# Performance work log

Measured on AMD Instinct MI355X. Metric: run time of the kernel, lower is better.

The kernel has to match this reference:

```python
import jax, jax.numpy as jnp
import numpy as np

B, T, C, H, DH, L, V = 4096, 32, 384, 6, 64, 6, 80


def _ln(x, g, b):
    m = x.mean(-1, keepdims=True)
    v = ((x - m) ** 2).mean(-1, keepdims=True)
    return (x - m) / jnp.sqrt(v + 1e-5) * g + b


def setup_inputs() -> dict:
    key = jax.random.key(0)
    ks = jax.random.split(key, 12)
    n = lambda k, s: jax.random.normal(k, s, dtype=jnp.float32) * 0.02
    return dict(
        idx=jax.random.randint(ks[0], (B, T), 0, V),
        tok_emb=n(ks[1], (V, C)),
        pos_emb=n(ks[2], (T, C)),
        ln1_g=jnp.ones((L, C), jnp.float32), ln1_b=jnp.zeros((L, C), jnp.float32),
        Wq=n(ks[3], (L, H, C, DH)), Wk=n(ks[4], (L, H, C, DH)), Wv=n(ks[5], (L, H, C, DH)),
        Wo=n(ks[6], (L, C, C)), bo=jnp.zeros((L, C), jnp.float32),
        ln2_g=jnp.ones((L, C), jnp.float32), ln2_b=jnp.zeros((L, C), jnp.float32),
        W1=n(ks[7], (L, C, 4 * C)), b1=jnp.zeros((L, 4 * C), jnp.float32),
        W2=n(ks[8], (L, 4 * C, C)), b2=jnp.zeros((L, C), jnp.float32),
        lnf_g=jnp.ones((C,), jnp.float32), lnf_b=jnp.zeros((C,), jnp.float32),
        Wlm=n(ks[9], (C, V)), blm=jnp.zeros((V,), jnp.float32),
    )


def reference(idx, tok_emb, pos_emb, ln1_g, ln1_b, Wq, Wk, Wv, Wo, bo,
              ln2_g, ln2_b, W1, b1, W2, b2, lnf_g, lnf_b, Wlm, blm):
    # token + position embeddings
    x = tok_emb[idx] + pos_emb[None]  # [B, T, C]
    mask = jnp.tril(jnp.ones((T, T), dtype=bool))  # causal

    def block(x, p):
        l1g, l1b, wq, wk, wv, wo, b_o, l2g, l2b, w1, b_1, w2, b_2 = p
        h = _ln(x, l1g, l1b)
        q = jnp.einsum('btc,hcd->bhtd', h, wq)
        k = jnp.einsum('btc,hcd->bhtd', h, wk)
        v = jnp.einsum('btc,hcd->bhtd', h, wv)
        s = jnp.einsum('bhtd,bhsd->bhts', q, k) * (DH ** -0.5)
        s = jnp.where(mask, s, -jnp.inf)
        a = jax.nn.softmax(s, axis=-1)  # dropout is identity in eval
        o = jnp.einsum('bhts,bhsd->bhtd', a, v)
        o = o.transpose(0, 2, 1, 3).reshape(x.shape[0], T, C)  # concat heads
        x = x + o @ wo + b_o
        h2 = _ln(x, l2g, l2b)
        x = x + jax.nn.relu(h2 @ w1 + b_1) @ w2 + b_2
        return x, None

    params = (ln1_g, ln1_b, Wq, Wk, Wv, Wo, bo, ln2_g, ln2_b, W1, b1, W2, b2)
    x, _ = jax.lax.scan(block, x, params)
    x = _ln(x, lnf_g, lnf_b)
    return x @ Wlm + blm  # [B, T, V]
```

## Files before the change

### kernel.cpp

```cpp
#include <hip/hip_runtime.h>
#include <hip/hip_fp16.h>
#include <stdint.h>


typedef unsigned short u16;
typedef __bf16 bf16x8 __attribute__((ext_vector_type(8)));
typedef float f32x4 __attribute__((ext_vector_type(4)));
typedef float f32x4v __attribute__((ext_vector_type(4)));
typedef unsigned uint2v __attribute__((ext_vector_type(2)));

#define M_TOK 131072
#define CDIM  384
#define TT    32
#define HH    6
#define DHEAD 64
#define LLAY  6
#define VOCAB 80
#define FFDIM 1536
#define QKVN  1152

__device__ __forceinline__ float b2f(u16 v) {
    union { unsigned int u; float f; } x; x.u = ((unsigned int)v) << 16; return x.f;
}
__device__ __forceinline__ u16 f2b(float f) {
    union { float f; unsigned int u; } x; x.f = f;
    unsigned int r = (x.u + 0x7fffu + ((x.u >> 16) & 1u)) >> 16;
    return (u16)r;
}
__device__ __forceinline__ void gload16(const u16* g, u16* l) {
    __builtin_amdgcn_global_load_lds(
        (const __attribute__((address_space(1))) void*)g,
        (__attribute__((address_space(3))) void*)l,
        16, 0, 0);
}
__device__ __forceinline__ float load_in(const void* p, size_t i, int m) {
    if (m == 0) return ((const float*)p)[i];
    u16 v = ((const u16*)p)[i];
    if (m == 1) return b2f(v);
    __half h; *(u16*)&h = v; return __half2float(h);
}

__global__ void detect_dtype_kernel(const void* ln1g, int* flag) {
    if (threadIdx.x == 0 && blockIdx.x == 0) {
        unsigned w = *(const unsigned*)ln1g;
        int m = 0;
        if (w == 0x3F803F80u) m = 1;
        else if (w == 0x3C003C00u) m = 2;
        *flag = m;
    }
}

__global__ void cvt_kernel(const void* __restrict__ src, u16* __restrict__ dst,
                           unsigned n, const int* __restrict__ flag) {
    const int m = *flag;
    unsigned i = blockIdx.x * 256 + threadIdx.x;
    if (i < n) dst[i] = f2b(load_in(src, i, m));
}

__global__ void transpose_kernel(const void* __restrict__ src, u16* __restrict__ dst,
                                 int R, int Cc, unsigned total,
                                 const int* __restrict__ flag) {
    const int m = *flag;
    unsigned i = blockIdx.x * 256 + threadIdx.x;
    if (i >= total) return;
    unsigned c  = i % R;
    unsigned t2 = i / R;
    unsigned n  = t2 % Cc;
    unsigned l  = t2 / Cc;
    dst[i] = f2b(load_in(src, ((size_t)l * R + c) * Cc + n, m));
}

__global__ void pack_qkv_kernel(const void* __restrict__ Wq, const void* __restrict__ Wk,
                                const void* __restrict__ Wv, u16* __restrict__ dst,
                                const int* __restrict__ flag) {
    const int m = *flag;
    unsigned i = blockIdx.x * 256 + threadIdx.x;
    const unsigned total = (unsigned)LLAY * QKVN * CDIM;
    if (i >= total) return;
    unsigned c  = i % CDIM;
    unsigned t2 = i / CDIM;
    unsigned n  = t2 % QKVN;
    unsigned l  = t2 / QKVN;
    const void* W = (n < 384) ? Wq : (n < 768) ? Wk : Wv;
    unsigned nn = n % 384;
    unsigned hh = nn >> 6, d = nn & 63;
    dst[i] = f2b(load_in(W, (((size_t)l * HH + hh) * CDIM + c) * DHEAD + d, m));
}

__global__ void embed_kernel(const int* __restrict__ idx, const void* __restrict__ tok,
                             const void* __restrict__ pos, u16* __restrict__ x,
                             unsigned rows0, const int* __restrict__ flag) {
    const int m = *flag;
    unsigned i = blockIdx.x * 256 + threadIdx.x;
    unsigned c  = i % CDIM;
    unsigned bt = i / CDIM + rows0;
    unsigned t  = bt & (TT - 1);
    int id = idx[bt];
    x[i] = f2b(load_in(tok, (size_t)id * CDIM + c, m) + load_in(pos, (size_t)t * CDIM + c, m));
}

__global__ __launch_bounds__(256) void ln_kernel(const u16* __restrict__ x,
                                                 const u16* __restrict__ g,
                                                 const u16* __restrict__ b,
                                                 u16* __restrict__ out) {
    const unsigned row  = blockIdx.x * 4 + (threadIdx.x >> 6);
    const unsigned lane = threadIdx.x & 63;
    const u16* xr = x + (size_t)row * CDIM;
    float v[8];
    float s = 0.f, s2 = 0.f;
    if (lane < 48) {
        uint4 xv = *(const uint4*)&xr[lane * 8];
        u16 xa[8]; *(uint4*)xa = xv;
#pragma unroll
        for (int j = 0; j < 8; j++) { v[j] = b2f(xa[j]); s += v[j]; s2 += v[j] * v[j]; }
    }
#pragma unroll
    for (int off = 32; off; off >>= 1) { s += __shfl_xor(s, off); s2 += __shfl_xor(s2, off); }
    const float mean = s * (1.f / CDIM);
    const float var  = fmaxf(s2 * (1.f / CDIM) - mean * mean, 0.f);
    const float rstd = rsqrtf(var + 1e-5f);
    if (lane < 48) {
        uint4 gv = *(const uint4*)(g + lane * 8);
        uint4 bv = *(const uint4*)(b + lane * 8);
        u16 ga[8], ba[8];
        *(uint4*)ga = gv; *(uint4*)ba = bv;
        uint4 o;
        unsigned ow[4];
#pragma unroll
        for (int p = 0; p < 4; p++) {
            const float h0 = (v[2 * p]     - mean) * rstd * b2f(ga[2 * p])     + b2f(ba[2 * p]);
            const float h1 = (v[2 * p + 1] - mean) * rstd * b2f(ga[2 * p + 1]) + b2f(ba[2 * p + 1]);
            ow[p] = (unsigned)f2b(h0) | ((unsigned)f2b(h1) << 16);
        }
        o.x = ow[0]; o.y = ow[1]; o.z = ow[2]; o.w = ow[3];
        *(uint4*)(out + (size_t)row * CDIM + lane * 8) = o;
    }
}

template<bool WIDE, bool BIAS, bool RELU, bool RESID, bool NBOUND, bool FOUT>
__global__ __launch_bounds__(512, WIDE ? 4 : 6)
void gemm_kernel(const u16* __restrict__ A, const u16* __restrict__ Bt,
                 const u16* __restrict__ bias, const u16* __restrict__ resid,
                 u16* __restrict__ Cb, float* Cf,
                 int N, int K, int nt) {
    constexpr int BN = WIDE ? 256 : 128;
    constexpr int NF = WIDE ? 4 : 2;
    constexpr int WC = BN / 4;
    constexpr int BI = BN / 64;
    __shared__ __align__(16) u16 smem[8192 + BN * 64];
    u16* As = smem;
    u16* Bs = smem + 8192;
    float* eps = (float*)smem;

    const int tid  = threadIdx.x;
    const int lane = tid & 63;
    const int w    = tid >> 6;
    const int quad = lane >> 4;
    const int l16  = lane & 15;
    const int wm = w >> 2, wn = w & 3;

    const int id = blockIdx.x;
    const int sgrp = id >> 3;
    const int mtile = (id & 7) + 8 * (sgrp / nt);
    const int ntile = sgrp % nt;
    const long m0 = (long)mtile * 128;
    const long n0 = (long)ntile * BN;

    const u16* Ag[2]; u16* ldsA[2];
    const u16* Bg[BI]; u16* ldsB[BI];
#pragma unroll
    for (int n = 0; n < 2; n++) {
        const int si  = w * 128 + n * 64 + lane;
        const int row = si >> 3;
        const int p   = si & 7;
        const int s   = p ^ (row & 7);
        Ag[n] = A + (size_t)(m0 + row) * K + s * 8;
        ldsA[n] = As + (size_t)(w * 128 + n * 64) * 8;
    }
#pragma unroll
    for (int n = 0; n < BI; n++) {
        const int si  = (w * BI + n) * 64 + lane;
        const int row = si >> 3;
        const int p   = si & 7;
        const int s   = p ^ (row & 7);
        long brow = n0 + row;
        if (NBOUND) brow = brow < N ? brow : N - 1;
        Bg[n] = Bt + (size_t)brow * K + s * 8;
        ldsB[n] = Bs + (size_t)((w * BI + n) * 64) * 8;
    }

    f32x4 acc[4][NF];
#pragma unroll
    for (int i = 0; i < 4; i++)
#pragma unroll
        for (int j = 0; j < NF; j++) acc[i][j] = f32x4{0.f, 0.f, 0.f, 0.f};

    for (int k0 = 0; k0 < K; k0 += 64) {
        __syncthreads();
#pragma unroll
        for (int n = 0; n < 2; n++)  gload16(Ag[n] + k0, ldsA[n]);
#pragma unroll
        for (int n = 0; n < BI; n++) gload16(Bg[n] + k0, ldsB[n]);
        __syncthreads();
#pragma unroll
        for (int k32 = 0; k32 < 2; k32++) {
            bf16x8 af[4], bfr[NF];
#pragma unroll
            for (int i = 0; i < 4; i++) {
                const int row = wm * 64 + i * 16 + l16;
                const int p   = (k32 * 4 + quad) ^ (row & 7);
                af[i] = *(const bf16x8*)(&As[row * 64 + p * 8]);
            }
#pragma unroll
            for (int j = 0; j < NF; j++) {
                const int row = wn * WC + j * 16 + l16;
                const int p   = (k32 * 4 + quad) ^ (row & 7);
                bfr[j] = *(const bf16x8*)(&Bs[row * 64 + p * 8]);
            }
#pragma unroll
            for (int i = 0; i < 4; i++)
#pragma unroll
                for (int j = 0; j < NF; j++)
                    acc[i][j] = __builtin_amdgcn_mfma_f32_16x16x32_bf16(af[i], bfr[j], acc[i][j], 0, 0, 0);
        }
    }

    float bv[NF];
#pragma unroll
    for (int j = 0; j < NF; j++) {
        if (BIAS) {
            int col = (int)n0 + wn * WC + j * 16 + l16;
            bv[j] = (!NBOUND || col < N) ? b2f(bias[col]) : 0.f;
        } else bv[j] = 0.f;
    }

    constexpr int SR  = WIDE ? 32 : 64;
    constexpr int NPH = 128 / SR;
    constexpr int IB  = SR / 16;
    constexpr int TPR = BN / 4;
    constexpr int RPP = 512 / TPR;
    const int cc = (tid & (TPR - 1)) * 4;
    const int rr = tid / TPR;
#pragma unroll
    for (int q = 0; q < NPH; q++) {
        __syncthreads();
        if (wm == (q * SR) / 64) {
            const int ibase = ((q * SR) % 64) / 16;
#pragma unroll
            for (int ii = 0; ii < IB; ii++)
#pragma unroll
                for (int j = 0; j < NF; j++) {
                    const int lr = ii * 16 + quad * 4;
                    const int lc = wn * WC + j * 16 + l16;
#pragma unroll
                    for (int r = 0; r < 4; r++) {
                        float v = acc[ibase + ii][j][r] + bv[j];
                        if (RELU) v = fmaxf(v, 0.f);
                        eps[(lr + r) * BN + lc] = v;
                    }
                }
        }
        __syncthreads();
        const long rowbase = m0 + q * SR;
#pragma unroll
        for (int p = 0; p < SR / RPP; p++) {
            const int lrow = p * RPP + rr;
            const long grow = rowbase + lrow;
            f32x4v v = *(const f32x4v*)&eps[lrow * BN + cc];
            const long col = n0 + cc;
            if (RESID) {
                if (!NBOUND || col + 3 < N) {
                    const uint2v rv = *(const uint2v*)&resid[grow * N + col];
                    v.x += b2f((u16)(rv.x & 0xffffu));
                    v.y += b2f((u16)(rv.x >> 16));
                    v.z += b2f((u16)(rv.y & 0xffffu));
                    v.w += b2f((u16)(rv.y >> 16));
                    uint2v pk;
                    pk.x = (unsigned)f2b(v.x) | ((unsigned)f2b(v.y) << 16);
                    pk.y = (unsigned)f2b(v.z) | ((unsigned)f2b(v.w) << 16);
                    *(uint2v*)&Cb[grow * N + col] = pk;
                }
            } else if (FOUT) {
                if (!NBOUND || col + 3 < N)
                    __builtin_nontemporal_store(v, (f32x4v*)&Cf[grow * N + col]);
            } else {
                if (!NBOUND || col + 3 < N) {
                    uint2v pk;
                    pk.x = (unsigned)f2b(v.x) | ((unsigned)f2b(v.y) << 16);
                    pk.y = (unsigned)f2b(v.z) | ((unsigned)f2b(v.w) << 16);
                    *(uint2v*)&Cb[grow * N + col] = pk;
                }
            }
        }
    }
}

__global__ __launch_bounds__(256, 2) void attn_kernel(const u16* __restrict__ qkv,
                                                      u16* __restrict__ o) {
    __shared__ __align__(16) u16 alds[4 * 3840];
    const int w    = threadIdx.x >> 6;
    u16* Pl = alds + w * 3840;
    u16* VT = Pl + 1280;

    const int gw   = blockIdx.x * 4 + w;
    const int seq  = gw / HH;
    const int h    = gw - seq * HH;
    const int lane = threadIdx.x & 63;
    const int l16  = lane & 15;
    const int quad = lane >> 4;

    const u16* base = qkv + (size_t)seq * TT * QKVN;
    const u16* Qb = base + h * DHEAD;
    const u16* Kb = base + 384 + h * DHEAD;
    const u16* Vb = base + 768 + h * DHEAD;

    {
        const int s  = lane & 31;
        const int hf = lane >> 5;
#pragma unroll
        for (int c = 0; c < 4; c++) {
            uint4 v = *(const uint4*)(Vb + (size_t)s * QKVN + hf * 32 + c * 8);
            const u16* pv = (const u16*)&v;
#pragma unroll
            for (int j = 0; j < 8; j++) {
                const int d = hf * 32 + c * 8 + j;
                VT[d * 40 + s] = pv[j];
            }
        }
    }

    bf16x8 qf[2][2], kf[2][2];
#pragma unroll
    for (int ti = 0; ti < 2; ti++)
#pragma unroll
        for (int kt = 0; kt < 2; kt++)
            qf[ti][kt] = *(const bf16x8*)(Qb + (size_t)(ti * 16 + l16) * QKVN + kt * 32 + quad * 8);
#pragma unroll
    for (int si = 0; si < 2; si++)
#pragma unroll
        for (int kt = 0; kt < 2; kt++)
            kf[si][kt] = *(const bf16x8*)(Kb + (size_t)(si * 16 + l16) * QKVN + kt * 32 + quad * 8);

    f32x4 S00 = f32x4{0.f, 0.f, 0.f, 0.f};
    f32x4 S10 = f32x4{0.f, 0.f, 0.f, 0.f};
    f32x4 S11 = f32x4{0.f, 0.f, 0.f, 0.f};
#pragma unroll
    for (int kt = 0; kt < 2; kt++) {
        S00 = __builtin_amdgcn_mfma_f32_16x16x32_bf16(qf[0][kt], kf[0][kt], S00, 0, 0, 0);
        S10 = __builtin_amdgcn_mfma_f32_16x16x32_bf16(qf[1][kt], kf[0][kt], S10, 0, 0, 0);
        S11 = __builtin_amdgcn_mfma_f32_16x16x32_bf16(qf[1][kt], kf[1][kt], S11, 0, 0, 0);
    }

#pragma unroll
    for (int ti = 0; ti < 2; ti++) {
#pragma unroll
        for (int r = 0; r < 4; r++) {
            const int t = ti * 16 + quad * 4 + r;
            float v0 = (ti ? S10[r] : S00[r]) * 0.125f;
            if (l16 > t) v0 = -1e30f;
            float v1 = -1e30f;
            if (ti == 1) {
                v1 = S11[r] * 0.125f;
                if (16 + l16 > t) v1 = -1e30f;
            }
            float m = fmaxf(v0, v1);
#pragma unroll
            for (int k = 1; k < 16; k <<= 1) m = fmaxf(m, __shfl_xor(m, k));
            const float e0 = __expf(v0 - m);
            const float e1 = (ti == 1) ? __expf(v1 - m) : 0.f;
            float l = e0 + e1;
#pragma unroll
            for (int k = 1; k < 16; k <<= 1) l += __shfl_xor(l, k);
            const float inv = 1.f / l;
            Pl[t * 40 + l16]      = f2b(e0 * inv);
            Pl[t * 40 + 16 + l16] = f2b(e1 * inv);
        }
    }

    bf16x8 pf[2], vf[4];
#pragma unroll
    for (int ti = 0; ti < 2; ti++)
        pf[ti] = *(const bf16x8*)(&Pl[(ti * 16 + l16) * 40 + quad * 8]);
#pragma unroll
    for (int dt = 0; dt < 4; dt++)
        vf[dt] = *(const bf16x8*)(&VT[(dt * 16 + l16) * 40 + quad * 8]);

    u16* ob = o + ((size_t)seq * TT) * CDIM + h * DHEAD;
#pragma unroll
    for (int ti = 0; ti < 2; ti++) {
#pragma unroll
        for (int dt = 0; dt < 4; dt++) {
            f32x4 O2 = f32x4{0.f, 0.f, 0.f, 0.f};
            O2 = __builtin_amdgcn_mfma_f32_16x16x32_bf16(pf[ti], vf[dt], O2, 0, 0, 0);
#pragma unroll
            for (int r = 0; r < 4; r++) {
                const int t = ti * 16 + quad * 4 + r;
                ob[(size_t)t * CDIM + dt * 16 + l16] = f2b(O2[r]);
            }
        }
    }
}

extern "C" void kernel_launch(void* const* d_in, const int* in_sizes, int n_in,
                              void* d_out, int out_size, void* d_ws, size_t ws_size,
                              hipStream_t stream) {
    const int*  idx  = (const int*)d_in[0];
    const void* tok  = d_in[1];
    const void* pos  = d_in[2];
    const void* ln1g = d_in[3];
    const void* ln1b = d_in[4];
    const void* Wq   = d_in[5];
    const void* Wk   = d_in[6];
    const void* Wv   = d_in[7];
    const void* Wo   = d_in[8];
    const void* bo   = d_in[9];
    const void* ln2g = d_in[10];
    const void* ln2b = d_in[11];
    const void* W1   = d_in[12];
    const void* b1   = d_in[13];
    const void* W2   = d_in[14];
    const void* b2   = d_in[15];
    const void* lnfg = d_in[16];
    const void* lnfb = d_in[17];
    const void* Wlm  = d_in[18];
    const void* blm  = d_in[19];

    const size_t wq_b  = (size_t)LLAY * QKVN * CDIM * 2;
    const size_t wo_b  = (size_t)LLAY * CDIM * CDIM * 2;
    const size_t w1_b  = (size_t)LLAY * FFDIM * CDIM * 2;
    const size_t w2_b  = (size_t)LLAY * CDIM * FFDIM * 2;
    const size_t wlm_b = (size_t)VOCAB * CDIM * 2;
    const size_t wts   = wq_b + wo_b + w1_b + w2_b + wlm_b;

    const unsigned P_LN1G = 0,      P_LN1B = 2304,  P_BO  = 4608;
    const unsigned P_LN2G = 6912,   P_LN2B = 9216,  P_B1  = 11520;
    const unsigned P_B2   = 20736,  P_LNFG = 23040, P_LNFB = 23424;
    const unsigned P_BLM  = 23808,  P_TOT  = 23888;
    const size_t pbuf_b = ((size_t)P_TOT * 2 + 255) & ~(size_t)255;

    int NC = 32;
    {
        const int cand[6] = {1, 2, 4, 8, 16, 32};
        for (int ci = 0; ci < 6; ci++) {
            size_t rows_c = (size_t)M_TOK / cand[ci];
            size_t need = rows_c * 5376 + wts + pbuf_b + 4096;
            if (need <= ws_size) { NC = cand[ci]; break; }
        }
    }
    const size_t rows = (size_t)M_TOK / NC;
    const int mt = (int)(rows / 128);

    char* ws = (char*)d_ws;
    size_t off = 0;
    u16*   x    = (u16*)(ws + off);   off += rows * CDIM * 4;
    u16*   h    = (u16*)(ws + off);   off += rows * CDIM * 2;
    char*  S    = ws + off;           off += rows * 3072;
    u16*   qkv  = (u16*)S;
    u16*   o    = (u16*)(S + rows * QKVN * 2);
    u16*   u    = (u16*)S;
    u16* wqkvT  = (u16*)(ws + off);   off += wq_b;
    u16* woT    = (u16*)(ws + off);   off += wo_b;
    u16* w1T    = (u16*)(ws + off);   off += w1_b;
    u16* w2T    = (u16*)(ws + off);   off += w2_b;
    u16* wlmT   = (u16*)(ws + off);   off += wlm_b;
    u16* pbuf   = (u16*)(ws + off);   off += pbuf_b;
    int* flag   = (int*)(ws + off);   off += 256;

    detect_dtype_kernel<<<1, 64, 0, stream>>>(ln1g, flag);

    struct { const void* src; unsigned doff, n; } cv[10] = {
        { ln1g, P_LN1G, 2304 }, { ln1b, P_LN1B, 2304 }, { bo, P_BO, 2304 },
        { ln2g, P_LN2G, 2304 }, { ln2b, P_LN2B, 2304 }, { b1, P_B1, 9216 },
        { b2,   P_B2,   2304 }, { lnfg, P_LNFG, 384 },  { lnfb, P_LNFB, 384 },
        { blm,  P_BLM,  80 },
    };
    for (int i = 0; i < 10; i++)
        cvt_kernel<<<(cv[i].n + 255) / 256, 256, 0, stream>>>(cv[i].src, pbuf + cv[i].doff, cv[i].n, flag);

    {
        unsigned tq = (unsigned)LLAY * QKVN * CDIM;
        pack_qkv_kernel<<<(tq + 255) / 256, 256, 0, stream>>>(Wq, Wk, Wv, wqkvT, flag);
        unsigned t1 = (unsigned)LLAY * CDIM * CDIM;
        transpose_kernel<<<(t1 + 255) / 256, 256, 0, stream>>>(Wo, woT, CDIM, CDIM, t1, flag);
        unsigned t2t = (unsigned)LLAY * CDIM * FFDIM;
        transpose_kernel<<<(t2t + 255) / 256, 256, 0, stream>>>(W1, w1T, CDIM, FFDIM, t2t, flag);
        transpose_kernel<<<(t2t + 255) / 256, 256, 0, stream>>>(W2, w2T, FFDIM, CDIM, t2t, flag);
        unsigned t3 = (unsigned)VOCAB * CDIM;
        transpose_kernel<<<(t3 + 255) / 256, 256, 0, stream>>>(Wlm, wlmT, CDIM, VOCAB, t3, flag);
    }

    for (int c = 0; c < NC; c++) {
        const size_t r0 = c * rows;
        embed_kernel<<<(rows * CDIM) / 256, 256, 0, stream>>>(idx, tok, pos, x, (unsigned)r0, flag);

        for (int l = 0; l < LLAY; l++) {
            ln_kernel<<<rows / 4, 256, 0, stream>>>(x, pbuf + P_LN1G + l * CDIM, pbuf + P_LN1B + l * CDIM, h);
            gemm_kernel<true, false, false, false, true, false><<<mt * 5, 512, 0, stream>>>(
                h, wqkvT + (size_t)l * QKVN * CDIM, nullptr, nullptr, qkv, nullptr, QKVN, CDIM, 5);
            attn_kernel<<<(rows / TT) * HH / 4, 256, 0, stream>>>(qkv, o);
            gemm_kernel<false, true, false, true, false, false><<<mt * 3, 512, 0, stream>>>(
                o, woT + (size_t)l * CDIM * CDIM, pbuf + P_BO + l * CDIM, x, x, nullptr, CDIM, CDIM, 3);
            ln_kernel<<<rows / 4, 256, 0, stream>>>(x, pbuf + P_LN2G + l * CDIM, pbuf + P_LN2B + l * CDIM, h);
            gemm_kernel<true, true, true, false, false, false><<<mt * 6, 512, 0, stream>>>(
                h, w1T + (size_t)l * FFDIM * CDIM, pbuf + P_B1 + l * FFDIM, nullptr, u, nullptr, FFDIM, CDIM, 6);
            gemm_kernel<false, true, false, true, false, false><<<mt * 3, 512, 0, stream>>>(
                u, w2T + (size_t)l * CDIM * FFDIM, pbuf + P_B2 + l * CDIM, x, x, nullptr, CDIM, FFDIM, 3);
        }

        ln_kernel<<<rows / 4, 256, 0, stream>>>(x, pbuf + P_LNFG, pbuf + P_LNFB, h);
        gemm_kernel<false, true, false, false, true, true><<<mt, 512, 0, stream>>>(
            h, wlmT, pbuf + P_BLM, nullptr, nullptr, (float*)d_out + r0 * VOCAB, VOCAB, CDIM, 1);
    }
}
```

Measured before the change: 5.160 ms.

## Fuse LayerNorm into residual GEMM epilogues and embedding kernel

```diff
diff --git a/kernel.cpp b/kernel.cpp
--- a/kernel.cpp
+++ b/kernel.cpp
@@ -87,32 +87,33 @@
     dst[i] = f2b(load_in(W, (((size_t)l * HH + hh) * CDIM + c) * DHEAD + d, m));
 }
 
-__global__ void embed_kernel(const int* __restrict__ idx, const void* __restrict__ tok,
-                             const void* __restrict__ pos, u16* __restrict__ x,
-                             unsigned rows0, const int* __restrict__ flag) {
+__global__ __launch_bounds__(256) void embed_ln_kernel(
+        const int* __restrict__ idx, const void* __restrict__ tok,
+        const void* __restrict__ pos, const u16* __restrict__ g,
+        const u16* __restrict__ b, u16* __restrict__ x, u16* __restrict__ h,
+        unsigned rows0, const int* __restrict__ flag) {
     const int m = *flag;
-    unsigned i = blockIdx.x * 256 + threadIdx.x;
-    unsigned c  = i % CDIM;
-    unsigned bt = i / CDIM + rows0;
-    unsigned t  = bt & (TT - 1);
-    int id = idx[bt];
-    x[i] = f2b(load_in(tok, (size_t)id * CDIM + c, m) + load_in(pos, (size_t)t * CDIM + c, m));
-}
-
-__global__ __launch_bounds__(256) void ln_kernel(const u16* __restrict__ x,
-                                                 const u16* __restrict__ g,
-                                                 const u16* __restrict__ b,
-                                                 u16* __restrict__ out) {
     const unsigned row  = blockIdx.x * 4 + (threadIdx.x >> 6);
     const unsigned lane = threadIdx.x & 63;
-    const u16* xr = x + (size_t)row * CDIM;
+    const unsigned bt = row + rows0;
+    const unsigned t  = bt & (TT - 1);
+    const int id = idx[bt];
     float v[8];
     float s = 0.f, s2 = 0.f;
     if (lane < 48) {
-        uint4 xv = *(const uint4*)&xr[lane * 8];
-        u16 xa[8]; *(uint4*)xa = xv;
-#pragma unroll
-        for (int j = 0; j < 8; j++) { v[j] = b2f(xa[j]); s += v[j]; s2 += v[j] * v[j]; }
+        unsigned ow[4];
+#pragma unroll
+        for (int j = 0; j < 8; j++) {
+            const unsigned c = lane * 8 + j;
+            v[j] = load_in(tok, (size_t)id * CDIM + c, m)
+                 + load_in(pos, (size_t)t * CDIM + c, m);
+            s += v[j]; s2 += v[j] * v[j];
+        }
+#pragma unroll
+        for (int p = 0; p < 4; p++)
+            ow[p] = (unsigned)f2b(v[2 * p]) | ((unsigned)f2b(v[2 * p + 1]) << 16);
+        uint4 o; o.x = ow[0]; o.y = ow[1]; o.z = ow[2]; o.w = ow[3];
+        *(uint4*)(x + (size_t)row * CDIM + lane * 8) = o;
     }
 #pragma unroll
     for (int off = 32; off; off >>= 1) { s += __shfl_xor(s, off); s2 += __shfl_xor(s2, off); }
@@ -124,7 +125,6 @@
         uint4 bv = *(const uint4*)(b + lane * 8);
         u16 ga[8], ba[8];
         *(uint4*)ga = gv; *(uint4*)ba = bv;
-        uint4 o;
         unsigned ow[4];
 #pragma unroll
         for (int p = 0; p < 4; p++) {
@@ -132,8 +132,8 @@
             const float h1 = (v[2 * p + 1] - mean) * rstd * b2f(ga[2 * p + 1]) + b2f(ba[2 * p + 1]);
             ow[p] = (unsigned)f2b(h0) | ((unsigned)f2b(h1) << 16);
         }
-        o.x = ow[0]; o.y = ow[1]; o.z = ow[2]; o.w = ow[3];
-        *(uint4*)(out + (size_t)row * CDIM + lane * 8) = o;
+        uint4 o; o.x = ow[0]; o.y = ow[1]; o.z = ow[2]; o.w = ow[3];
+        *(uint4*)(h + (size_t)row * CDIM + lane * 8) = o;
     }
 }
 
@@ -295,6 +295,156 @@
     }
 }
 
+__global__ __launch_bounds__(512, 2)
+void gemm_n384ln_kernel(const u16* __restrict__ A, const u16* __restrict__ Bt,
+                        const u16* __restrict__ bias, u16* __restrict__ x,
+                        const u16* __restrict__ lng, const u16* __restrict__ lnb,
+                        u16* __restrict__ hout, int K) {
+    __shared__ __align__(16) u16 smem[28672];
+    u16* As = smem;
+    u16* Bs = smem + 4096;
+    float* eps = (float*)smem;
+
+    const int tid  = threadIdx.x;
+    const int lane = tid & 63;
+    const int w    = tid >> 6;
+    const int quad = lane >> 4;
+    const int l16  = lane & 15;
+    const long m0  = (long)blockIdx.x * 64;
+
+    const int arow = tid >> 3;
+    const int as_  = (tid & 7) ^ (arow & 7);
+    const u16* Ag = A + (size_t)(m0 + arow) * K + as_ * 8;
+    u16* ldsA = As + (size_t)(w * 64) * 8;
+
+    const u16* Bg[6]; u16* ldsB[6];
+#pragma unroll
+    for (int n = 0; n < 6; n++) {
+        const int si  = n * 512 + tid;
+        const int row = si >> 3;
+        const int s   = (si & 7) ^ (row & 7);
+        Bg[n]   = Bt + (size_t)row * K + s * 8;
+        ldsB[n] = Bs + (size_t)(n * 512 + w * 64) * 8;
+    }
+
+    f32x4 acc[4][3];
+#pragma unroll
+    for (int i = 0; i < 4; i++)
+#pragma unroll
+        for (int j = 0; j < 3; j++) acc[i][j] = f32x4{0.f, 0.f, 0.f, 0.f};
+
+    for (int k0 = 0; k0 < K; k0 += 64) {
+        __syncthreads();
+        gload16(Ag + k0, ldsA);
+#pragma unroll
+        for (int n = 0; n < 6; n++) gload16(Bg[n] + k0, ldsB[n]);
+        __syncthreads();
+#pragma unroll
+        for (int k32 = 0; k32 < 2; k32++) {
+            bf16x8 af[4], bfr[3];
+#pragma unroll
+            for (int i = 0; i < 4; i++) {
+                const int row = i * 16 + l16;
+                const int p   = (k32 * 4 + quad) ^ (row & 7);
+                af[i] = *(const bf16x8*)(&As[row * 64 + p * 8]);
+            }
+#pragma unroll
+            for (int j = 0; j < 3; j++) {
+                const int row = w * 48 + j * 16 + l16;
+                const int p   = (k32 * 4 + quad) ^ (row & 7);
+                bfr[j] = *(const bf16x8*)(&Bs[row * 64 + p * 8]);
+            }
+#pragma unroll
+            for (int i = 0; i < 4; i++)
+#pragma unroll
+                for (int j = 0; j < 3; j++)
+                    acc[i][j] = __builtin_amdgcn_mfma_f32_16x16x32_bf16(af[i], bfr[j], acc[i][j], 0, 0, 0);
+        }
+    }
+
+    float bv[3];
+#pragma unroll
+    for (int j = 0; j < 3; j++) bv[j] = b2f(bias[w * 48 + j * 16 + l16]);
+
+#pragma unroll
+    for (int q = 0; q < 2; q++) {
+        __syncthreads();
+#pragma unroll
+        for (int i2 = 0; i2 < 2; i2++) {
+            const int i  = q * 2 + i2;
+            const int lr = i2 * 16 + quad * 4;
+            const int lc = w * 48;
+#pragma unroll
+            for (int j = 0; j < 3; j++)
+#pragma unroll
+                for (int r = 0; r < 4; r++)
+                    eps[(lr + r) * 384 + lc + j * 16 + l16] = acc[i][j][r] + bv[j];
+        }
+        __syncthreads();
+        const long rowbase = m0 + q * 32;
+#pragma unroll
+        for (int p = 0; p < 6; p++) {
+            const int idxp = p * 512 + tid;
+            const int lrow = idxp / 96;
+            const int c4   = (idxp % 96) * 4;
+            f32x4v v = *(const f32x4v*)&eps[lrow * 384 + c4];
+            const long grow = rowbase + lrow;
+            const uint2v rv = *(const uint2v*)&x[grow * 384 + c4];
+            v.x += b2f((u16)(rv.x & 0xffffu));
+            v.y += b2f((u16)(rv.x >> 16));
+            v.z += b2f((u16)(rv.y & 0xffffu));
+            v.w += b2f((u16)(rv.y >> 16));
+            uint2v pk;
+            pk.x = (unsigned)f2b(v.x) | ((unsigned)f2b(v.y) << 16);
+            pk.y = (unsigned)f2b(v.z) | ((unsigned)f2b(v.w) << 16);
+            *(uint2v*)&x[grow * 384 + c4] = pk;
+            *(f32x4v*)&eps[lrow * 384 + c4] = v;
+        }
+        __syncthreads();
+        {
+            const int srow = w * 4 + (lane >> 4);
+            const int c0   = l16 * 24;
+            float vv[24];
+            float s = 0.f, s2 = 0.f;
+#pragma unroll
+            for (int k = 0; k < 6; k++) {
+                const f32x4v t4 = *(const f32x4v*)&eps[srow * 384 + c0 + k * 4];
+                vv[k * 4 + 0] = t4.x; vv[k * 4 + 1] = t4.y;
+                vv[k * 4 + 2] = t4.z; vv[k * 4 + 3] = t4.w;
+                s  += t4.x + t4.y + t4.z + t4.w;
+                s2 += t4.x * t4.x + t4.y * t4.y + t4.z * t4.z + t4.w * t4.w;
+            }
+#pragma unroll
+            for (int off = 1; off < 16; off <<= 1) {
+                s += __shfl_xor(s, off); s2 += __shfl_xor(s2, off);
+            }
+            const float mean = s * (1.f / CDIM);
+            const float var  = fmaxf(s2 * (1.f / CDIM) - mean * mean, 0.f);
+            const float rstd = rsqrtf(var + 1e-5f);
+            u16 ga[24], ba[24];
+#pragma unroll
+            for (int k = 0; k < 3; k++) {
+                *(uint4*)&ga[k * 8] = *(const uint4*)(lng + c0 + k * 8);
+                *(uint4*)&ba[k * 8] = *(const uint4*)(lnb + c0 + k * 8);
+            }
+            unsigned ow[12];
+#pragma unroll
+            for (int p = 0; p < 12; p++) {
+                const float h0 = (vv[2 * p]     - mean) * rstd * b2f(ga[2 * p])     + b2f(ba[2 * p]);
+                const float h1 = (vv[2 * p + 1] - mean) * rstd * b2f(ga[2 * p + 1]) + b2f(ba[2 * p + 1]);
+                ow[p] = (unsigned)f2b(h0) | ((unsigned)f2b(h1) << 16);
+            }
+            u16* hp = hout + (size_t)(rowbase + srow) * 384 + c0;
+#pragma unroll
+            for (int k = 0; k < 3; k++) {
+                uint4 o; o.x = ow[k * 4]; o.y = ow[k * 4 + 1];
+                o.z = ow[k * 4 + 2]; o.w = ow[k * 4 + 3];
+                *(uint4*)(hp + k * 8) = o;
+            }
+        }
+    }
+}
+
 __global__ __launch_bounds__(256, 2) void attn_kernel(const u16* __restrict__ qkv,
                                                       u16* __restrict__ o) {
     __shared__ __align__(16) u16 alds[4 * 3840];
@@ -449,6 +599,7 @@
     }
     const size_t rows = (size_t)M_TOK / NC;
     const int mt = (int)(rows / 128);
+    const int mt64 = (int)(rows / 64);
 
     char* ws = (char*)d_ws;
     size_t off = 0;
@@ -491,23 +642,25 @@
 
     for (int c = 0; c < NC; c++) {
         const size_t r0 = c * rows;
-        embed_kernel<<<(rows * CDIM) / 256, 256, 0, stream>>>(idx, tok, pos, x, (unsigned)r0, flag);
+        embed_ln_kernel<<<rows / 4, 256, 0, stream>>>(
+            idx, tok, pos, pbuf + P_LN1G, pbuf + P_LN1B, x, h, (unsigned)r0, flag);
 
         for (int l = 0; l < LLAY; l++) {
-            ln_kernel<<<rows / 4, 256, 0, stream>>>(x, pbuf + P_LN1G + l * CDIM, pbuf + P_LN1B + l * CDIM, h);
             gemm_kernel<true, false, false, false, true, false><<<mt * 5, 512, 0, stream>>>(
                 h, wqkvT + (size_t)l * QKVN * CDIM, nullptr, nullptr, qkv, nullptr, QKVN, CDIM, 5);
             attn_kernel<<<(rows / TT) * HH / 4, 256, 0, stream>>>(qkv, o);
-            gemm_kernel<false, true, false, true, false, false><<<mt * 3, 512, 0, stream>>>(
-                o, woT + (size_t)l * CDIM * CDIM, pbuf + P_BO + l * CDIM, x, x, nullptr, CDIM, CDIM, 3);
-            ln_kernel<<<rows / 4, 256, 0, stream>>>(x, pbuf + P_LN2G + l * CDIM, pbuf + P_LN2B + l * CDIM, h);
+            gemm_n384ln_kernel<<<mt64, 512, 0, stream>>>(
+                o, woT + (size_t)l * CDIM * CDIM, pbuf + P_BO + l * CDIM, x,
+                pbuf + P_LN2G + l * CDIM, pbuf + P_LN2B + l * CDIM, h, CDIM);
             gemm_kernel<true, true, true, false, false, false><<<mt * 6, 512, 0, stream>>>(
                 h, w1T + (size_t)l * FFDIM * CDIM, pbuf + P_B1 + l * FFDIM, nullptr, u, nullptr, FFDIM, CDIM, 6);
-            gemm_kernel<false, true, false, true, false, false><<<mt * 3, 512, 0, stream>>>(
-                u, w2T + (size_t)l * CDIM * FFDIM, pbuf + P_B2 + l * CDIM, x, x, nullptr, CDIM, FFDIM, 3);
-        }
-
-        ln_kernel<<<rows / 4, 256, 0, stream>>>(x, pbuf + P_LNFG, pbuf + P_LNFB, h);
+            const u16* ng = (l < LLAY - 1) ? (pbuf + P_LN1G + (l + 1) * CDIM) : (pbuf + P_LNFG);
+            const u16* nb = (l < LLAY - 1) ? (pbuf + P_LN1B + (l + 1) * CDIM) : (pbuf + P_LNFB);
+            gemm_n384ln_kernel<<<mt64, 512, 0, stream>>>(
+                u, w2T + (size_t)l * CDIM * FFDIM, pbuf + P_B2 + l * CDIM, x,
+                ng, nb, h, FFDIM);
+        }
+
         gemm_kernel<false, true, false, false, true, true><<<mt, 512, 0, stream>>>(
             h, wlmT, pbuf + P_BLM, nullptr, nullptr, (float*)d_out + r0 * VOCAB, VOCAB, CDIM, 1);
     }
```

After: 6.201 ms. +20.2%, slower.
